# Optimization experiments

Measured on AMD Instinct MI355X. Metric: run time of the kernel, lower is better.

The kernel has to match this reference:

```python
import jax, jax.numpy as jnp
import numpy as np

V, H_BASE, D, L, K = 32000, 4096, 512, 2, 4
B = 64

def setup_inputs() -> dict:
    key = jax.random.key(0)
    ks = jax.random.split(key, 12)
    s = 0.02
    return {
        "hidden_state": jax.random.normal(ks[0], (B, H_BASE), jnp.float32),
        "in_proj_w": jax.random.normal(ks[1], (D, H_BASE), jnp.float32) * s,
        "in_proj_b": jnp.zeros((D,), jnp.float32),
        "w_ih0": jax.random.normal(ks[2], (3 * D, D), jnp.float32) * s,
        "w_hh0": jax.random.normal(ks[3], (3 * D, D), jnp.float32) * s,
        "b_ih0": jax.random.normal(ks[4], (3 * D,), jnp.float32) * s,
        "b_hh0": jax.random.normal(ks[5], (3 * D,), jnp.float32) * s,
        "w_ih1": jax.random.normal(ks[6], (3 * D, D), jnp.float32) * s,
        "w_hh1": jax.random.normal(ks[7], (3 * D, D), jnp.float32) * s,
        "b_ih1": jax.random.normal(ks[8], (3 * D,), jnp.float32) * s,
        "b_hh1": jax.random.normal(ks[9], (3 * D,), jnp.float32) * s,
        "embed": jax.random.normal(ks[10], (V, D), jnp.float32) * s,
        "out_w": jax.random.normal(ks[11], (V, D), jnp.float32) * s,
    }

def _gru_cell(x, h, w_ih, w_hh, b_ih, b_hh):
    # PyTorch GRU gate order: r, z, n
    gi = x @ w_ih.T + b_ih  # [B, 3D]
    gh = h @ w_hh.T + b_hh
    ir, iz, inn = jnp.split(gi, 3, axis=-1)
    hr, hz, hn = jnp.split(gh, 3, axis=-1)
    r = jax.nn.sigmoid(ir + hr)
    z = jax.nn.sigmoid(iz + hz)
    n = jnp.tanh(inn + r * hn)
    return (1.0 - z) * n + z * h

def reference(hidden_state, in_proj_w, in_proj_b, w_ih0, w_hh0, b_ih0, b_hh0,
              w_ih1, w_hh1, b_ih1, b_hh1, embed, out_w):
    b = hidden_state.shape[0]
    h0 = hidden_state @ in_proj_w.T + in_proj_b  # [B, D]
    h_l0 = h0
    h_l1 = h0
    x = jnp.zeros((b, in_proj_w.shape[0]), hidden_state.dtype)
    all_logits = []
    for _ in range(K):
        h_l0 = _gru_cell(x, h_l0, w_ih0, w_hh0, b_ih0, b_hh0)
        h_l1 = _gru_cell(h_l0, h_l1, w_ih1, w_hh1, b_ih1, b_hh1)
        logits = h_l1 @ out_w.T  # [B, V]
        all_logits.append(logits)
        x = embed[jnp.argmax(logits, axis=-1)]  # greedy next-token embed
    return jnp.stack(all_logits, axis=1)  # [B, K, V]
```

## Files before the change

kernel.cpp:

```cpp
#include <hip/hip_runtime.h>
#include <math.h>


typedef __attribute__((ext_vector_type(8))) short short8;
typedef __attribute__((ext_vector_type(4))) float f32x4;

__device__ __forceinline__ unsigned short f2bf_rne(float x) {
    unsigned u = __float_as_uint(x);
    unsigned r = (u + 0x7fffu + ((u >> 16) & 1u)) >> 16;
    return (unsigned short)r;
}
__device__ __forceinline__ void split2(float x, unsigned short& hi, unsigned short& lo) {
    unsigned u = __float_as_uint(x);
    hi = (unsigned short)(u >> 16);
    float r = x - __uint_as_float(u & 0xffff0000u);
    lo = f2bf_rne(r);
}

__device__ __forceinline__ void store_plane(unsigned short* hiP, unsigned short* loP,
                                            int m, int d, float v) {
    int s = d >> 6, cl = (d >> 3) & 7, e = d & 7;
    int off = m * 512 + s * 64 + ((cl ^ (m & 7)) * 8) + e;
    unsigned short hi, lo; split2(v, hi, lo);
    hiP[off] = hi; loP[off] = lo;
}

__device__ __forceinline__ void gload16(const void* g, void* lds) {
    __builtin_amdgcn_global_load_lds(
        (const __attribute__((address_space(1))) unsigned int*)g,
        (__attribute__((address_space(3))) unsigned int*)lds, 16, 0, 0);
}

__device__ __forceinline__ void split_w_body(
    const float* __restrict__ W, unsigned short* __restrict__ H,
    unsigned short* __restrict__ L, size_t g, int kclog)
{
    int n  = (int)(g >> kclog);
    int c8 = (int)g & ((1 << kclog) - 1);
    const float* src = W + g * 8;
    float4 v0 = *(const float4*)src;
    float4 v1 = *(const float4*)(src + 4);
    unsigned short h[8], l[8];
    split2(v0.x,h[0],l[0]); split2(v0.y,h[1],l[1]); split2(v0.z,h[2],l[2]); split2(v0.w,h[3],l[3]);
    split2(v1.x,h[4],l[4]); split2(v1.y,h[5],l[5]); split2(v1.z,h[6],l[6]); split2(v1.w,h[7],l[7]);
    uint4 ph = make_uint4((unsigned)h[0]|((unsigned)h[1]<<16), (unsigned)h[2]|((unsigned)h[3]<<16),
                          (unsigned)h[4]|((unsigned)h[5]<<16), (unsigned)h[6]|((unsigned)h[7]<<16));
    uint4 pl = make_uint4((unsigned)l[0]|((unsigned)l[1]<<16), (unsigned)l[2]|((unsigned)l[3]<<16),
                          (unsigned)l[4]|((unsigned)l[5]<<16), (unsigned)l[6]|((unsigned)l[7]<<16));
    int nt = n >> 7, row = n & 127;
    int ksi = c8 >> 3;
    int slot = (c8 & 7) ^ (row & 7);
    int tpr = 1 << (kclog - 3);
    size_t off = ((size_t)(nt * tpr + ksi) * 128 + row) * 64 + slot * 8;
    *(uint4*)(H + off) = ph;
    *(uint4*)(L + off) = pl;
}

__global__ __launch_bounds__(256) void k_split_W(
    const float* __restrict__ W, unsigned short* __restrict__ H,
    unsigned short* __restrict__ L, int kclog)
{
    size_t g = (size_t)blockIdx.x * 256 + threadIdx.x;
    split_w_body(W, H, L, g, kclog);
}

__global__ __launch_bounds__(256) void k_split_gw(
    const float* __restrict__ w0, const float* __restrict__ w1,
    const float* __restrict__ w2, const float* __restrict__ w3,
    unsigned short* __restrict__ H, unsigned short* __restrict__ L)
{
    int mat = blockIdx.y;
    const float* W = mat == 0 ? w0 : mat == 1 ? w1 : mat == 2 ? w2 : w3;
    size_t g = (size_t)blockIdx.x * 256 + threadIdx.x;
    split_w_body(W, H + (size_t)mat * 786432, L + (size_t)mat * 786432, g, 6);
}

template<bool ARGMAX>
__device__ __forceinline__ void mfma_gemm(
    const char* __restrict__ AH, const char* __restrict__ AL, int AstrideB, int akk0,
    const unsigned short* __restrict__ BH, const unsigned short* __restrict__ BL,
    size_t btileU,
    int nk,
    float* __restrict__ C, int ldc, int n0,
    unsigned short (*AsH)[4096], unsigned short (*AsL)[4096],
    unsigned short (*BsH)[8192], unsigned short (*BsL)[8192],
    float* __restrict__ pval, int* __restrict__ pidx, int bx)
{
    const int tid  = threadIdx.x;
    const int wv   = tid >> 6;
    const int lane = tid & 63;
    const int lr   = lane & 15;
    const int lh   = lane >> 4;
    const int m    = tid >> 3;
    const int cp   = tid & 7;

    f32x4 acc[4];
#pragma unroll
    for (int i = 0; i < 4; ++i) acc[i] = (f32x4){0.f, 0.f, 0.f, 0.f};

    auto stage = [&](int t, int p) {
        const int ka = (akk0 + t * 64) * 2;
        gload16(AH + m * AstrideB + ka + cp * 16, (char*)AsH[p] + wv * 1024);
        gload16(AL + m * AstrideB + ka + cp * 16, (char*)AsL[p] + wv * 1024);
        const char* bH = (const char*)BH + (btileU + (size_t)t * 8192) * 2;
        const char* bL = (const char*)BL + (btileU + (size_t)t * 8192) * 2;
        gload16(bH + wv * 2048 +        lane * 16, (char*)BsH[p] + wv * 2048);
        gload16(bH + wv * 2048 + 1024 + lane * 16, (char*)BsH[p] + wv * 2048 + 1024);
        gload16(bL + wv * 2048 +        lane * 16, (char*)BsL[p] + wv * 2048);
        gload16(bL + wv * 2048 + 1024 + lane * 16, (char*)BsL[p] + wv * 2048 + 1024);
    };

    stage(0, 0);
    __syncthreads();

    for (int t = 0; t < nk; ++t) {
        const int p = t & 1;
        if (t + 1 < nk) stage(t + 1, p ^ 1);
#pragma unroll
        for (int kk2 = 0; kk2 < 2; ++kk2) {
            int aoff = lr * 64 + (((kk2 * 4 + lh) ^ (lr & 7)) * 8);
            short8 ah[4], al[4];
#pragma unroll
            for (int mt = 0; mt < 4; ++mt) {
                ah[mt] = *(const short8*)(AsH[p] + mt * 1024 + aoff);
                al[mt] = *(const short8*)(AsL[p] + mt * 1024 + aoff);
            }
            int brow = wv * 16 + lr;
            int boff = brow * 64 + (((kk2 * 4 + lh) ^ (brow & 7)) * 8);
            short8 bh = *(const short8*)(BsH[p] + boff);
            short8 bl = *(const short8*)(BsL[p] + boff);
#pragma unroll
            for (int mt = 0; mt < 4; ++mt) {
                acc[mt] = __builtin_amdgcn_mfma_f32_16x16x32_bf16(ah[mt], bh, acc[mt], 0, 0, 0);
                acc[mt] = __builtin_amdgcn_mfma_f32_16x16x32_bf16(ah[mt], bl, acc[mt], 0, 0, 0);
                acc[mt] = __builtin_amdgcn_mfma_f32_16x16x32_bf16(al[mt], bh, acc[mt], 0, 0, 0);
            }
        }
        __syncthreads();
    }

#pragma unroll
    for (int mt = 0; mt < 4; ++mt)
#pragma unroll
        for (int i = 0; i < 4; ++i) {
            int mm = mt * 16 + lh * 4 + i;
            C[mm * ldc + n0 + wv * 16 + lr] = acc[mt][i];
        }

    if (ARGMAX) {
        float* sv = (float*)&AsH[0][0];
        int*   sc = (int*)&AsL[0][0];
#pragma unroll
        for (int mt = 0; mt < 4; ++mt)
#pragma unroll
            for (int i = 0; i < 4; ++i) {
                float v = acc[mt][i];
                int   c = n0 + wv * 16 + lr;
#pragma unroll
                for (int msk = 1; msk < 16; msk <<= 1) {
                    float ov = __shfl_xor(v, msk, 64);
                    int   oc = __shfl_xor(c, msk, 64);
                    if (ov > v || (ov == v && oc < c)) { v = ov; c = oc; }
                }
                if (lr == 0) {
                    int row = mt * 16 + lh * 4 + i;
                    sv[wv * 64 + row] = v;
                    sc[wv * 64 + row] = c;
                }
            }
        __syncthreads();
        if (tid < 64) {
            float v = sv[tid]; int c = sc[tid];
#pragma unroll
            for (int w = 1; w < 8; ++w) {
                float ov = sv[w * 64 + tid]; int oc = sc[w * 64 + tid];
                if (ov > v) { v = ov; c = oc; }
            }
            pval[bx * 64 + tid] = v;
            pidx[bx * 64 + tid] = c;
        }
    }
}

#define DECLARE_LDS() \
    __shared__ alignas(16) unsigned short AsH[2][4096]; \
    __shared__ alignas(16) unsigned short AsL[2][4096]; \
    __shared__ alignas(16) unsigned short BsH[2][8192]; \
    __shared__ alignas(16) unsigned short BsL[2][8192];

__global__ __launch_bounds__(256) void k_split_A(
    const float* __restrict__ hidden, char* __restrict__ hidH, char* __restrict__ hidL)
{
    int g = blockIdx.x * 256 + threadIdx.x;
    int m = g >> 9;
    int cc = g & 511;
    int s = cc >> 3, cl = cc & 7;
    const float* src = hidden + m * 4096 + cc * 8;
    float4 v0 = *(const float4*)src;
    float4 v1 = *(const float4*)(src + 4);
    unsigned short h[8], l[8];
    split2(v0.x,h[0],l[0]); split2(v0.y,h[1],l[1]); split2(v0.z,h[2],l[2]); split2(v0.w,h[3],l[3]);
    split2(v1.x,h[4],l[4]); split2(v1.y,h[5],l[5]); split2(v1.z,h[6],l[6]); split2(v1.w,h[7],l[7]);
    uint4 ph = make_uint4((unsigned)h[0]|((unsigned)h[1]<<16), (unsigned)h[2]|((unsigned)h[3]<<16),
                          (unsigned)h[4]|((unsigned)h[5]<<16), (unsigned)h[6]|((unsigned)h[7]<<16));
    uint4 pl = make_uint4((unsigned)l[0]|((unsigned)l[1]<<16), (unsigned)l[2]|((unsigned)l[3]<<16),
                          (unsigned)l[4]|((unsigned)l[5]<<16), (unsigned)l[6]|((unsigned)l[7]<<16));
    int off = m * 8192 + s * 128 + ((cl ^ (m & 7)) * 16);
    *(uint4*)(hidH + off) = ph;
    *(uint4*)(hidL + off) = pl;
}

__global__ __launch_bounds__(512) void k_inproj(
    const char* __restrict__ hidH, const char* __restrict__ hidL,
    const unsigned short* __restrict__ WH, const unsigned short* __restrict__ WL,
    float* __restrict__ part)
{
    DECLARE_LDS();
    int nt = blockIdx.x & 3;
    int ks = blockIdx.x >> 2;
    mfma_gemm<false>(hidH, hidL, 8192, ks * 256,
                     WH, WL, (size_t)(nt * 64 + ks * 4) * 8192, 4,
                     part + ks * 32768, 512, nt * 128,
                     AsH, AsL, BsH, BsL, nullptr, nullptr, 0);
}

__global__ __launch_bounds__(256) void k_reduce_inproj(
    const float* __restrict__ part, const float* __restrict__ bias,
    float* __restrict__ hA, float* __restrict__ hB,
    unsigned short* hAH, unsigned short* hAL,
    unsigned short* hBH, unsigned short* hBL,
    unsigned short* xH,  unsigned short* xL)
{
    int i = blockIdx.x * 256 + threadIdx.x;
    int b = i >> 9;
    int d = i & 511;
    float s = bias[d];
#pragma unroll
    for (int ks = 0; ks < 16; ++ks) s += part[ks * 32768 + i];
    hA[i] = s;
    hB[i] = s;
    store_plane(hAH, hAL, b, d, s);
    store_plane(hBH, hBL, b, d, s);
    store_plane(xH,  xL,  b, d, 0.f);
}

__global__ __launch_bounds__(512) void k_gates(
    const char* __restrict__ xH, const char* __restrict__ xL,
    const char* __restrict__ hH, const char* __restrict__ hL,
    const unsigned short* __restrict__ gwH, const unsigned short* __restrict__ gwL,
    int layer, float* __restrict__ gip, float* __restrict__ ghp)
{
    DECLARE_LDS();
    int bx  = blockIdx.x;
    int nt  = bx % 12;
    int ks  = (bx / 12) & 3;
    int mat = bx / 48;
    const char* AH = mat ? hH : xH;
    const char* AL = mat ? hL : xL;
    float* C = (mat ? ghp : gip) + ks * 98304;
    size_t btile = ((size_t)(layer * 2 + mat) * 96 + nt * 8 + ks * 2) * 8192;
    mfma_gemm<false>(AH, AL, 1024, ks * 128,
                     gwH, gwL, btile, 2,
                     C, 1536, nt * 128,
                     AsH, AsL, BsH, BsL, nullptr, nullptr, 0);
}

__global__ __launch_bounds__(256) void k_combine(
    const float* __restrict__ gip, const float* __restrict__ ghp,
    const float* __restrict__ b_ih, const float* __restrict__ b_hh,
    float* __restrict__ h, unsigned short* hH, unsigned short* hL)
{
    int i = blockIdx.x * 256 + threadIdx.x;
    int b = i >> 9;
    int d = i & 511;
    int base = b * 1536 + d;
    float ir = b_ih[d], iz = b_ih[d + 512], inn = b_ih[d + 1024];
    float hr = b_hh[d], hz = b_hh[d + 512], hn = b_hh[d + 1024];
#pragma unroll
    for (int ks = 0; ks < 4; ++ks) {
        const float* gi = gip + ks * 98304 + base;
        const float* gh = ghp + ks * 98304 + base;
        ir  += gi[0];    iz += gi[512];  inn += gi[1024];
        hr  += gh[0];    hz += gh[512];  hn  += gh[1024];
    }
    float r = 1.f / (1.f + expf(-(ir + hr)));
    float z = 1.f / (1.f + expf(-(iz + hz)));
    float n = tanhf(inn + r * hn);
    float hv = (1.f - z) * n + z * h[i];
    h[i] = hv;
    store_plane(hH, hL, b, d, hv);
}

__global__ __launch_bounds__(512) void k_logits(
    const char* __restrict__ hH, const char* __restrict__ hL,
    const unsigned short* __restrict__ WH, const unsigned short* __restrict__ WL,
    float* __restrict__ out, int step,
    float* __restrict__ pval, int* __restrict__ pidx)
{
    DECLARE_LDS();
    mfma_gemm<true>(hH, hL, 1024, 0,
                    WH, WL, (size_t)blockIdx.x * 8 * 8192, 8,
                    out + step * 32000, 128000, blockIdx.x * 128,
                    AsH, AsL, BsH, BsL, pval, pidx, blockIdx.x);
}

__global__ __launch_bounds__(256) void k_reduce_embed(
    const float* __restrict__ pval, const int* __restrict__ pidx,
    const float* __restrict__ embed, unsigned short* xH, unsigned short* xL)
{
    __shared__ float sv[256];
    __shared__ int   sc[256];
    const int b = blockIdx.x;
    const int tid = threadIdx.x;
    float v = -3.4e38f;
    int   c = 0x7fffffff;
    if (tid < 250) { v = pval[tid * 64 + b]; c = pidx[tid * 64 + b]; }
    sv[tid] = v; sc[tid] = c;
    __syncthreads();
    for (int s = 128; s > 0; s >>= 1) {
        if (tid < s) {
            float ov = sv[tid + s]; int oc = sc[tid + s];
            if (ov > sv[tid] || (ov == sv[tid] && oc < sc[tid])) { sv[tid] = ov; sc[tid] = oc; }
        }
        __syncthreads();
    }
    int tok = sc[0];
    for (int j = tid; j < 512; j += 256)
        store_plane(xH, xL, b, j, embed[tok * 512 + j]);
}

extern "C" void kernel_launch(void* const* d_in, const int* in_sizes, int n_in,
                              void* d_out, int out_size, void* d_ws, size_t ws_size,
                              hipStream_t stream)
{
    const float* hidden = (const float*)d_in[0];
    const float* in_w   = (const float*)d_in[1];
    const float* in_b   = (const float*)d_in[2];
    const float* w_ih0  = (const float*)d_in[3];
    const float* w_hh0  = (const float*)d_in[4];
    const float* b_ih0  = (const float*)d_in[5];
    const float* b_hh0  = (const float*)d_in[6];
    const float* w_ih1  = (const float*)d_in[7];
    const float* w_hh1  = (const float*)d_in[8];
    const float* b_ih1  = (const float*)d_in[9];
    const float* b_hh1  = (const float*)d_in[10];
    const float* embed  = (const float*)d_in[11];
    const float* out_w  = (const float*)d_in[12];
    float* out = (float*)d_out;
    char*  ws  = (char*)d_ws;

    float* hA  = (float*)(ws + 0);
    float* hB  = (float*)(ws + 131072);
    unsigned short* xH  = (unsigned short*)(ws + 262144);
    unsigned short* xL  = (unsigned short*)(ws + 327680);
    unsigned short* hAH = (unsigned short*)(ws + 393216);
    unsigned short* hAL = (unsigned short*)(ws + 458752);
    unsigned short* hBH = (unsigned short*)(ws + 524288);
    unsigned short* hBL = (unsigned short*)(ws + 589824);
    char* hidH = ws + 655360;
    char* hidL = ws + 1179648;
    float* gip = (float*)(ws + 1703936);
    float* ghp = (float*)(ws + 3276800);
    float* pval = (float*)(ws + 4849664);
    int*   pidx = (int*)  (ws + 4913664);
    float* ipart = (float*)(ws + 4980736);
    unsigned short* owH = (unsigned short*)(ws + 8388608);
    unsigned short* owL = (unsigned short*)(ws + 41943040);
    unsigned short* gwH = (unsigned short*)(ws + 75497472);
    unsigned short* gwL = (unsigned short*)(ws + 83886080);
    unsigned short* inH = (unsigned short*)(ws + 92274688);
    unsigned short* inL = (unsigned short*)(ws + 96468992);

    k_split_A<<<128, 256, 0, stream>>>(hidden, hidH, hidL);
    k_split_W<<<8000, 256, 0, stream>>>(out_w, owH, owL, 6);
    k_split_gw<<<dim3(384, 4), 256, 0, stream>>>(w_ih0, w_hh0, w_ih1, w_hh1, gwH, gwL);
    k_split_W<<<1024, 256, 0, stream>>>(in_w, inH, inL, 9);
    k_inproj<<<64, 512, 0, stream>>>(hidH, hidL, inH, inL, ipart);
    k_reduce_inproj<<<128, 256, 0, stream>>>(ipart, in_b, hA, hB,
                                             hAH, hAL, hBH, hBL, xH, xL);

    for (int step = 0; step < 4; ++step) {
        k_gates<<<96, 512, 0, stream>>>((char*)xH, (char*)xL, (char*)hAH, (char*)hAL,
                                        gwH, gwL, 0, gip, ghp);
        k_combine<<<128, 256, 0, stream>>>(gip, ghp, b_ih0, b_hh0, hA, hAH, hAL);
        k_gates<<<96, 512, 0, stream>>>((char*)hAH, (char*)hAL, (char*)hBH, (char*)hBL,
                                        gwH, gwL, 1, gip, ghp);
        k_combine<<<128, 256, 0, stream>>>(gip, ghp, b_ih1, b_hh1, hB, hBH, hBL);
        k_logits<<<250, 512, 0, stream>>>((char*)hBH, (char*)hBL, owH, owL,
                                          out, step, pval, pidx);
        k_reduce_embed<<<64, 256, 0, stream>>>(pval, pidx, embed, xH, xL);
    }
}
```

Measured before the change: 361.9 us.

## Fuse all launches into one cooperative persistent kernel with grid syncs

Replaces the chain of about 30 kernel launches (weight splits, in-proj, gates, combine, logits, argmax/embed per step) with one cooperative kernel of 256 blocks separated by grid.sync. It also re-splits the K dimension more finely (64-way in-proj, 8-way gates) to use more blocks per phase, and overlaps the out_w and GRU weight splitting with the in-proj GEMM. The aim is to remove launch gaps and fill more CUs. The cost is grid-wide barriers, idle blocks in small phases, and larger partial-sum reductions.

```diff
diff --git a/kernel.cpp b/kernel.cpp
--- a/kernel.cpp
+++ b/kernel.cpp
@@ -1,6 +1,9 @@
 #include <hip/hip_runtime.h>
+#include <hip/hip_cooperative_groups.h>
 #include <math.h>
 
+
+namespace cg = cooperative_groups;
 
 typedef __attribute__((ext_vector_type(8))) short short8;
 typedef __attribute__((ext_vector_type(4))) float f32x4;
@@ -56,142 +59,10 @@
     *(uint4*)(L + off) = pl;
 }
 
-__global__ __launch_bounds__(256) void k_split_W(
-    const float* __restrict__ W, unsigned short* __restrict__ H,
-    unsigned short* __restrict__ L, int kclog)
-{
-    size_t g = (size_t)blockIdx.x * 256 + threadIdx.x;
-    split_w_body(W, H, L, g, kclog);
-}
-
-__global__ __launch_bounds__(256) void k_split_gw(
-    const float* __restrict__ w0, const float* __restrict__ w1,
-    const float* __restrict__ w2, const float* __restrict__ w3,
-    unsigned short* __restrict__ H, unsigned short* __restrict__ L)
-{
-    int mat = blockIdx.y;
-    const float* W = mat == 0 ? w0 : mat == 1 ? w1 : mat == 2 ? w2 : w3;
-    size_t g = (size_t)blockIdx.x * 256 + threadIdx.x;
-    split_w_body(W, H + (size_t)mat * 786432, L + (size_t)mat * 786432, g, 6);
-}
-
-template<bool ARGMAX>
-__device__ __forceinline__ void mfma_gemm(
-    const char* __restrict__ AH, const char* __restrict__ AL, int AstrideB, int akk0,
-    const unsigned short* __restrict__ BH, const unsigned short* __restrict__ BL,
-    size_t btileU,
-    int nk,
-    float* __restrict__ C, int ldc, int n0,
-    unsigned short (*AsH)[4096], unsigned short (*AsL)[4096],
-    unsigned short (*BsH)[8192], unsigned short (*BsL)[8192],
-    float* __restrict__ pval, int* __restrict__ pidx, int bx)
-{
-    const int tid  = threadIdx.x;
-    const int wv   = tid >> 6;
-    const int lane = tid & 63;
-    const int lr   = lane & 15;
-    const int lh   = lane >> 4;
-    const int m    = tid >> 3;
-    const int cp   = tid & 7;
-
-    f32x4 acc[4];
-#pragma unroll
-    for (int i = 0; i < 4; ++i) acc[i] = (f32x4){0.f, 0.f, 0.f, 0.f};
-
-    auto stage = [&](int t, int p) {
-        const int ka = (akk0 + t * 64) * 2;
-        gload16(AH + m * AstrideB + ka + cp * 16, (char*)AsH[p] + wv * 1024);
-        gload16(AL + m * AstrideB + ka + cp * 16, (char*)AsL[p] + wv * 1024);
-        const char* bH = (const char*)BH + (btileU + (size_t)t * 8192) * 2;
-        const char* bL = (const char*)BL + (btileU + (size_t)t * 8192) * 2;
-        gload16(bH + wv * 2048 +        lane * 16, (char*)BsH[p] + wv * 2048);
-        gload16(bH + wv * 2048 + 1024 + lane * 16, (char*)BsH[p] + wv * 2048 + 1024);
-        gload16(bL + wv * 2048 +        lane * 16, (char*)BsL[p] + wv * 2048);
-        gload16(bL + wv * 2048 + 1024 + lane * 16, (char*)BsL[p] + wv * 2048 + 1024);
-    };
-
-    stage(0, 0);
-    __syncthreads();
-
-    for (int t = 0; t < nk; ++t) {
-        const int p = t & 1;
-        if (t + 1 < nk) stage(t + 1, p ^ 1);
-#pragma unroll
-        for (int kk2 = 0; kk2 < 2; ++kk2) {
-            int aoff = lr * 64 + (((kk2 * 4 + lh) ^ (lr & 7)) * 8);
-            short8 ah[4], al[4];
-#pragma unroll
-            for (int mt = 0; mt < 4; ++mt) {
-                ah[mt] = *(const short8*)(AsH[p] + mt * 1024 + aoff);
-                al[mt] = *(const short8*)(AsL[p] + mt * 1024 + aoff);
-            }
-            int brow = wv * 16 + lr;
-            int boff = brow * 64 + (((kk2 * 4 + lh) ^ (brow & 7)) * 8);
-            short8 bh = *(const short8*)(BsH[p] + boff);
-            short8 bl = *(const short8*)(BsL[p] + boff);
-#pragma unroll
-            for (int mt = 0; mt < 4; ++mt) {
-                acc[mt] = __builtin_amdgcn_mfma_f32_16x16x32_bf16(ah[mt], bh, acc[mt], 0, 0, 0);
-                acc[mt] = __builtin_amdgcn_mfma_f32_16x16x32_bf16(ah[mt], bl, acc[mt], 0, 0, 0);
-                acc[mt] = __builtin_amdgcn_mfma_f32_16x16x32_bf16(al[mt], bh, acc[mt], 0, 0, 0);
-            }
-        }
-        __syncthreads();
-    }
-
-#pragma unroll
-    for (int mt = 0; mt < 4; ++mt)
-#pragma unroll
-        for (int i = 0; i < 4; ++i) {
-            int mm = mt * 16 + lh * 4 + i;
-            C[mm * ldc + n0 + wv * 16 + lr] = acc[mt][i];
-        }
-
-    if (ARGMAX) {
-        float* sv = (float*)&AsH[0][0];
-        int*   sc = (int*)&AsL[0][0];
-#pragma unroll
-        for (int mt = 0; mt < 4; ++mt)
-#pragma unroll
-            for (int i = 0; i < 4; ++i) {
-                float v = acc[mt][i];
-                int   c = n0 + wv * 16 + lr;
-#pragma unroll
-                for (int msk = 1; msk < 16; msk <<= 1) {
-                    float ov = __shfl_xor(v, msk, 64);
-                    int   oc = __shfl_xor(c, msk, 64);
-                    if (ov > v || (ov == v && oc < c)) { v = ov; c = oc; }
-                }
-                if (lr == 0) {
-                    int row = mt * 16 + lh * 4 + i;
-                    sv[wv * 64 + row] = v;
-                    sc[wv * 64 + row] = c;
-                }
-            }
-        __syncthreads();
-        if (tid < 64) {
-            float v = sv[tid]; int c = sc[tid];
-#pragma unroll
-            for (int w = 1; w < 8; ++w) {
-                float ov = sv[w * 64 + tid]; int oc = sc[w * 64 + tid];
-                if (ov > v) { v = ov; c = oc; }
-            }
-            pval[bx * 64 + tid] = v;
-            pidx[bx * 64 + tid] = c;
-        }
-    }
-}
-
-#define DECLARE_LDS() \
-    __shared__ alignas(16) unsigned short AsH[2][4096]; \
-    __shared__ alignas(16) unsigned short AsL[2][4096]; \
-    __shared__ alignas(16) unsigned short BsH[2][8192]; \
-    __shared__ alignas(16) unsigned short BsL[2][8192];
-
-__global__ __launch_bounds__(256) void k_split_A(
-    const float* __restrict__ hidden, char* __restrict__ hidH, char* __restrict__ hidL)
-{
-    int g = blockIdx.x * 256 + threadIdx.x;
+__device__ __forceinline__ void split_a_body(
+    const float* __restrict__ hidden, char* __restrict__ hidH,
+    char* __restrict__ hidL, int g)
+{
     int m = g >> 9;
     int cc = g & 511;
     int s = cc >> 3, cl = cc & 7;
@@ -210,144 +81,132 @@
     *(uint4*)(hidL + off) = pl;
 }
 
-__global__ __launch_bounds__(512) void k_inproj(
-    const char* __restrict__ hidH, const char* __restrict__ hidL,
-    const unsigned short* __restrict__ WH, const unsigned short* __restrict__ WL,
-    float* __restrict__ part)
-{
-    DECLARE_LDS();
-    int nt = blockIdx.x & 3;
-    int ks = blockIdx.x >> 2;
-    mfma_gemm<false>(hidH, hidL, 8192, ks * 256,
-                     WH, WL, (size_t)(nt * 64 + ks * 4) * 8192, 4,
-                     part + ks * 32768, 512, nt * 128,
-                     AsH, AsL, BsH, BsL, nullptr, nullptr, 0);
-}
-
-__global__ __launch_bounds__(256) void k_reduce_inproj(
-    const float* __restrict__ part, const float* __restrict__ bias,
-    float* __restrict__ hA, float* __restrict__ hB,
-    unsigned short* hAH, unsigned short* hAL,
-    unsigned short* hBH, unsigned short* hBL,
-    unsigned short* xH,  unsigned short* xL)
-{
-    int i = blockIdx.x * 256 + threadIdx.x;
-    int b = i >> 9;
-    int d = i & 511;
-    float s = bias[d];
-#pragma unroll
-    for (int ks = 0; ks < 16; ++ks) s += part[ks * 32768 + i];
-    hA[i] = s;
-    hB[i] = s;
-    store_plane(hAH, hAL, b, d, s);
-    store_plane(hBH, hBL, b, d, s);
-    store_plane(xH,  xL,  b, d, 0.f);
-}
-
-__global__ __launch_bounds__(512) void k_gates(
-    const char* __restrict__ xH, const char* __restrict__ xL,
-    const char* __restrict__ hH, const char* __restrict__ hL,
-    const unsigned short* __restrict__ gwH, const unsigned short* __restrict__ gwL,
-    int layer, float* __restrict__ gip, float* __restrict__ ghp)
-{
-    DECLARE_LDS();
-    int bx  = blockIdx.x;
-    int nt  = bx % 12;
-    int ks  = (bx / 12) & 3;
-    int mat = bx / 48;
-    const char* AH = mat ? hH : xH;
-    const char* AL = mat ? hL : xL;
-    float* C = (mat ? ghp : gip) + ks * 98304;
-    size_t btile = ((size_t)(layer * 2 + mat) * 96 + nt * 8 + ks * 2) * 8192;
-    mfma_gemm<false>(AH, AL, 1024, ks * 128,
-                     gwH, gwL, btile, 2,
-                     C, 1536, nt * 128,
-                     AsH, AsL, BsH, BsL, nullptr, nullptr, 0);
-}
-
-__global__ __launch_bounds__(256) void k_combine(
-    const float* __restrict__ gip, const float* __restrict__ ghp,
-    const float* __restrict__ b_ih, const float* __restrict__ b_hh,
-    float* __restrict__ h, unsigned short* hH, unsigned short* hL)
-{
-    int i = blockIdx.x * 256 + threadIdx.x;
-    int b = i >> 9;
-    int d = i & 511;
-    int base = b * 1536 + d;
-    float ir = b_ih[d], iz = b_ih[d + 512], inn = b_ih[d + 1024];
-    float hr = b_hh[d], hz = b_hh[d + 512], hn = b_hh[d + 1024];
-#pragma unroll
-    for (int ks = 0; ks < 4; ++ks) {
-        const float* gi = gip + ks * 98304 + base;
-        const float* gh = ghp + ks * 98304 + base;
-        ir  += gi[0];    iz += gi[512];  inn += gi[1024];
-        hr  += gh[0];    hz += gh[512];  hn  += gh[1024];
-    }
-    float r = 1.f / (1.f + expf(-(ir + hr)));
-    float z = 1.f / (1.f + expf(-(iz + hz)));
-    float n = tanhf(inn + r * hn);
-    float hv = (1.f - z) * n + z * h[i];
-    h[i] = hv;
-    store_plane(hH, hL, b, d, hv);
-}
-
-__global__ __launch_bounds__(512) void k_logits(
-    const char* __restrict__ hH, const char* __restrict__ hL,
-    const unsigned short* __restrict__ WH, const unsigned short* __restrict__ WL,
-    float* __restrict__ out, int step,
-    float* __restrict__ pval, int* __restrict__ pidx)
-{
-    DECLARE_LDS();
-    mfma_gemm<true>(hH, hL, 1024, 0,
-                    WH, WL, (size_t)blockIdx.x * 8 * 8192, 8,
-                    out + step * 32000, 128000, blockIdx.x * 128,
-                    AsH, AsL, BsH, BsL, pval, pidx, blockIdx.x);
-}
-
-__global__ __launch_bounds__(256) void k_reduce_embed(
-    const float* __restrict__ pval, const int* __restrict__ pidx,
-    const float* __restrict__ embed, unsigned short* xH, unsigned short* xL)
-{
-    __shared__ float sv[256];
-    __shared__ int   sc[256];
-    const int b = blockIdx.x;
+template<bool ARGMAX>
+__device__ __forceinline__ void mfma_gemm(
+    const char* __restrict__ AH, const char* __restrict__ AL, int AstrideB, int akk0,
+    const unsigned short* __restrict__ BH, const unsigned short* __restrict__ BL,
+    size_t btileU, int nk,
+    float* __restrict__ C, int ldc, int n0,
+    unsigned short (*AsH)[4096], unsigned short (*AsL)[4096],
+    unsigned short (*BsH)[8192], unsigned short (*BsL)[8192],
+    float* __restrict__ pval, int* __restrict__ pidx, int bx)
+{
+    const int tid  = threadIdx.x;
+    const int wv   = tid >> 6;
+    const int lane = tid & 63;
+    const int lr   = lane & 15;
+    const int lh   = lane >> 4;
+    const int m    = tid >> 3;
+    const int cp   = tid & 7;
+
+    f32x4 acc[4];
+#pragma unroll
+    for (int i = 0; i < 4; ++i) acc[i] = (f32x4){0.f, 0.f, 0.f, 0.f};
+
+    auto stage = [&](int t, int p) {
+        const int ka = (akk0 + t * 64) * 2;
+        gload16(AH + m * AstrideB + ka + cp * 16, (char*)AsH[p] + wv * 1024);
+        gload16(AL + m * AstrideB + ka + cp * 16, (char*)AsL[p] + wv * 1024);
+        const char* bH = (const char*)BH + (btileU + (size_t)t * 8192) * 2;
+        const char* bL = (const char*)BL + (btileU + (size_t)t * 8192) * 2;
+        gload16(bH + wv * 2048 +        lane * 16, (char*)BsH[p] + wv * 2048);
+        gload16(bH + wv * 2048 + 1024 + lane * 16, (char*)BsH[p] + wv * 2048 + 1024);
+        gload16(bL + wv * 2048 +        lane * 16, (char*)BsL[p] + wv * 2048);
+        gload16(bL + wv * 2048 + 1024 + lane * 16, (char*)BsL[p] + wv * 2048 + 1024);
+    };
+
+    stage(0, 0);
+    __syncthreads();
+
+    for (int t = 0; t < nk; ++t) {
+        const int p = t & 1;
+        if (t + 1 < nk) stage(t + 1, p ^ 1);
+#pragma unroll
+        for (int kk2 = 0; kk2 < 2; ++kk2) {
+            int aoff = lr * 64 + (((kk2 * 4 + lh) ^ (lr & 7)) * 8);
+            short8 ah[4], al[4];
+#pragma unroll
+            for (int mt = 0; mt < 4; ++mt) {
+                ah[mt] = *(const short8*)(AsH[p] + mt * 1024 + aoff);
+                al[mt] = *(const short8*)(AsL[p] + mt * 1024 + aoff);
+            }
+            int brow = wv * 16 + lr;
+            int boff = brow * 64 + (((kk2 * 4 + lh) ^ (brow & 7)) * 8);
+            short8 bh = *(const short8*)(BsH[p] + boff);
+            short8 bl = *(const short8*)(BsL[p] + boff);
+#pragma unroll
+            for (int mt = 0; mt < 4; ++mt) {
+                acc[mt] = __builtin_amdgcn_mfma_f32_16x16x32_bf16(ah[mt], bh, acc[mt], 0, 0, 0);
+                acc[mt] = __builtin_amdgcn_mfma_f32_16x16x32_bf16(ah[mt], bl, acc[mt], 0, 0, 0);
+                acc[mt] = __builtin_amdgcn_mfma_f32_16x16x32_bf16(al[mt], bh, acc[mt], 0, 0, 0);
+            }
+        }
+        __syncthreads();
+    }
+
+#pragma unroll
+    for (int mt = 0; mt < 4; ++mt)
+#pragma unroll
+        for (int i = 0; i < 4; ++i) {
+            int mm = mt * 16 + lh * 4 + i;
+            C[mm * ldc + n0 + wv * 16 + lr] = acc[mt][i];
+        }
+
+    if (ARGMAX) {
+        float* sv = (float*)&AsH[0][0];
+        int*   sc = (int*)&AsL[0][0];
+#pragma unroll
+        for (int mt = 0; mt < 4; ++mt)
+#pragma unroll
+            for (int i = 0; i < 4; ++i) {
+                float v = acc[mt][i];
+                int   c = n0 + wv * 16 + lr;
+#pragma unroll
+                for (int msk = 1; msk < 16; msk <<= 1) {
+                    float ov = __shfl_xor(v, msk, 64);
+                    int   oc = __shfl_xor(c, msk, 64);
+                    if (ov > v || (ov == v && oc < c)) { v = ov; c = oc; }
+                }
+                if (lr == 0) {
+                    int row = mt * 16 + lh * 4 + i;
+                    sv[wv * 64 + row] = v;
+                    sc[wv * 64 + row] = c;
+                }
+            }
+        __syncthreads();
+        if (tid < 64) {
+            float v = sv[tid]; int c = sc[tid];
+#pragma unroll
+            for (int w = 1; w < 8; ++w) {
+                float ov = sv[w * 64 + tid]; int oc = sc[w * 64 + tid];
+                if (ov > v) { v = ov; c = oc; }
+            }
+            pval[bx * 64 + tid] = v;
+            pidx[bx * 64 + tid] = c;
+        }
+        __syncthreads();
+    }
+}
+
+struct KP {
+    const float *hidden, *in_w, *in_b, *w_ih0, *w_hh0, *b_ih0, *b_hh0,
+                *w_ih1, *w_hh1, *b_ih1, *b_hh1, *embed, *out_w;
+    float* out;
+    char* ws;
+};
+
+__global__ __launch_bounds__(512) void k_persistent(KP p)
+{
+    cg::grid_group grid = cg::this_grid();
+
+    __shared__ alignas(16) unsigned short AsH[2][4096];
+    __shared__ alignas(16) unsigned short AsL[2][4096];
+    __shared__ alignas(16) unsigned short BsH[2][8192];
+    __shared__ alignas(16) unsigned short BsL[2][8192];
+
+    const int bx  = blockIdx.x;
     const int tid = threadIdx.x;
-    float v = -3.4e38f;
-    int   c = 0x7fffffff;
-    if (tid < 250) { v = pval[tid * 64 + b]; c = pidx[tid * 64 + b]; }
-    sv[tid] = v; sc[tid] = c;
-    __syncthreads();
-    for (int s = 128; s > 0; s >>= 1) {
-        if (tid < s) {
-            float ov = sv[tid + s]; int oc = sc[tid + s];
-            if (ov > sv[tid] || (ov == sv[tid] && oc < sc[tid])) { sv[tid] = ov; sc[tid] = oc; }
-        }
-        __syncthreads();
-    }
-    int tok = sc[0];
-    for (int j = tid; j < 512; j += 256)
-        store_plane(xH, xL, b, j, embed[tok * 512 + j]);
-}
-
-extern "C" void kernel_launch(void* const* d_in, const int* in_sizes, int n_in,
-                              void* d_out, int out_size, void* d_ws, size_t ws_size,
-                              hipStream_t stream)
-{
-    const float* hidden = (const float*)d_in[0];
-    const float* in_w   = (const float*)d_in[1];
-    const float* in_b   = (const float*)d_in[2];
-    const float* w_ih0  = (const float*)d_in[3];
-    const float* w_hh0  = (const float*)d_in[4];
-    const float* b_ih0  = (const float*)d_in[5];
-    const float* b_hh0  = (const float*)d_in[6];
-    const float* w_ih1  = (const float*)d_in[7];
-    const float* w_hh1  = (const float*)d_in[8];
-    const float* b_ih1  = (const float*)d_in[9];
-    const float* b_hh1  = (const float*)d_in[10];
-    const float* embed  = (const float*)d_in[11];
-    const float* out_w  = (const float*)d_in[12];
-    float* out = (float*)d_out;
-    char*  ws  = (char*)d_ws;
+    char* ws = p.ws;
 
     float* hA  = (float*)(ws + 0);
     float* hB  = (float*)(ws + 131072);
@@ -360,34 +219,153 @@
     char* hidH = ws + 655360;
     char* hidL = ws + 1179648;
     float* gip = (float*)(ws + 1703936);
-    float* ghp = (float*)(ws + 3276800);
-    float* pval = (float*)(ws + 4849664);
-    int*   pidx = (int*)  (ws + 4913664);
-    float* ipart = (float*)(ws + 4980736);
-    unsigned short* owH = (unsigned short*)(ws + 8388608);
-    unsigned short* owL = (unsigned short*)(ws + 41943040);
-    unsigned short* gwH = (unsigned short*)(ws + 75497472);
-    unsigned short* gwL = (unsigned short*)(ws + 83886080);
-    unsigned short* inH = (unsigned short*)(ws + 92274688);
-    unsigned short* inL = (unsigned short*)(ws + 96468992);
-
-    k_split_A<<<128, 256, 0, stream>>>(hidden, hidH, hidL);
-    k_split_W<<<8000, 256, 0, stream>>>(out_w, owH, owL, 6);
-    k_split_gw<<<dim3(384, 4), 256, 0, stream>>>(w_ih0, w_hh0, w_ih1, w_hh1, gwH, gwL);
-    k_split_W<<<1024, 256, 0, stream>>>(in_w, inH, inL, 9);
-    k_inproj<<<64, 512, 0, stream>>>(hidH, hidL, inH, inL, ipart);
-    k_reduce_inproj<<<128, 256, 0, stream>>>(ipart, in_b, hA, hB,
-                                             hAH, hAL, hBH, hBL, xH, xL);
+    float* ghp = (float*)(ws + 4849664);
+    float* pval = (float*)(ws + 7995392);
+    int*   pidx = (int*)  (ws + 8059392);
+    float* ipart = (float*)(ws + 8388608);
+    unsigned short* owH = (unsigned short*)(ws + 16777216);
+    unsigned short* owL = (unsigned short*)(ws + 49545216);
+    unsigned short* gwH = (unsigned short*)(ws + 82313216);
+    unsigned short* gwL = (unsigned short*)(ws + 88604672);
+    unsigned short* inH = (unsigned short*)(ws + 94896128);
+    unsigned short* inL = (unsigned short*)(ws + 99090432);
+
+    const size_t gt = (size_t)bx * 512 + tid;
+
+    for (size_t g = gt; g < 262144; g += 131072)
+        split_w_body(p.in_w, inH, inL, g, 9);
+    if (gt < 32768)
+        split_a_body(p.hidden, hidH, hidL, (int)gt);
+    grid.sync();
+
+    {
+        int nt = bx & 3, ks = bx >> 2;
+        mfma_gemm<false>(hidH, hidL, 8192, ks * 64,
+                         inH, inL, (size_t)(nt * 64 + ks) * 8192, 1,
+                         ipart + ks * 32768, 512, nt * 128,
+                         AsH, AsL, BsH, BsL, nullptr, nullptr, 0);
+    }
+    for (size_t g = gt; g < 2048000; g += 131072)
+        split_w_body(p.out_w, owH, owL, g, 6);
+    for (size_t g = gt; g < 393216; g += 131072) {
+        int mat = (int)(g / 98304);
+        const float* W = mat == 0 ? p.w_ih0 : mat == 1 ? p.w_hh0
+                       : mat == 2 ? p.w_ih1 : p.w_hh1;
+        split_w_body(W, gwH + (size_t)mat * 786432, gwL + (size_t)mat * 786432,
+                     g % 98304, 6);
+    }
+    grid.sync();
+
+    if (bx < 64) {
+        int i = bx * 512 + tid;
+        int b = i >> 9, d = i & 511;
+        float s = p.in_b[d];
+        for (int ks = 0; ks < 64; ++ks) s += ipart[ks * 32768 + i];
+        hA[i] = s; hB[i] = s;
+        store_plane(hAH, hAL, b, d, s);
+        store_plane(hBH, hBL, b, d, s);
+        store_plane(xH,  xL,  b, d, 0.f);
+    }
+    grid.sync();
 
     for (int step = 0; step < 4; ++step) {
-        k_gates<<<96, 512, 0, stream>>>((char*)xH, (char*)xL, (char*)hAH, (char*)hAL,
-                                        gwH, gwL, 0, gip, ghp);
-        k_combine<<<128, 256, 0, stream>>>(gip, ghp, b_ih0, b_hh0, hA, hAH, hAL);
-        k_gates<<<96, 512, 0, stream>>>((char*)hAH, (char*)hAL, (char*)hBH, (char*)hBL,
-                                        gwH, gwL, 1, gip, ghp);
-        k_combine<<<128, 256, 0, stream>>>(gip, ghp, b_ih1, b_hh1, hB, hBH, hBL);
-        k_logits<<<250, 512, 0, stream>>>((char*)hBH, (char*)hBL, owH, owL,
-                                          out, step, pval, pidx);
-        k_reduce_embed<<<64, 256, 0, stream>>>(pval, pidx, embed, xH, xL);
-    }
-}
+#pragma unroll 1
+        for (int layer = 0; layer < 2; ++layer) {
+            if (bx < 192) {
+                int nt = bx % 12, ks = (bx / 12) & 7, mat = bx / 96;
+                const char* AH_;
+                const char* AL_;
+                if (layer == 0) { AH_ = mat ? (char*)hAH : (char*)xH;
+                                  AL_ = mat ? (char*)hAL : (char*)xL; }
+                else            { AH_ = mat ? (char*)hBH : (char*)hAH;
+                                  AL_ = mat ? (char*)hBL : (char*)hAL; }
+                float* C = (mat ? ghp : gip) + ks * 98304;
+                size_t btile = ((size_t)(layer * 2 + mat) * 96 + nt * 8 + ks) * 8192;
+                mfma_gemm<false>(AH_, AL_, 1024, ks * 64,
+                                 gwH, gwL, btile, 1,
+                                 C, 1536, nt * 128,
+                                 AsH, AsL, BsH, BsL, nullptr, nullptr, 0);
+            }
+            grid.sync();
+
+            if (bx < 64) {
+                int i = bx * 512 + tid;
+                int b = i >> 9, d = i & 511;
+                const float* bi = layer ? p.b_ih1 : p.b_ih0;
+                const float* bh2 = layer ? p.b_hh1 : p.b_hh0;
+                float ir = bi[d], iz = bi[d + 512], inn = bi[d + 1024];
+                float hr = bh2[d], hz = bh2[d + 512], hn = bh2[d + 1024];
+                int base = b * 1536 + d;
+#pragma unroll
+                for (int ks = 0; ks < 8; ++ks) {
+                    const float* gi = gip + ks * 98304 + base;
+                    const float* gh = ghp + ks * 98304 + base;
+                    ir += gi[0]; iz += gi[512]; inn += gi[1024];
+                    hr += gh[0]; hz += gh[512]; hn  += gh[1024];
+                }
+                float r = 1.f / (1.f + expf(-(ir + hr)));
+                float z = 1.f / (1.f + expf(-(iz + hz)));
+                float n = tanhf(inn + r * hn);
+                float* h = layer ? hB : hA;
+                float hv = (1.f - z) * n + z * h[i];
+                h[i] = hv;
+                store_plane(layer ? hBH : hAH, layer ? hBL : hAL, b, d, hv);
+            }
+            grid.sync();
+        }
+
+        if (bx < 250) {
+            mfma_gemm<true>((const char*)hBH, (const char*)hBL, 1024, 0,
+                            owH, owL, (size_t)bx * 8 * 8192, 8,
+                            p.out + step * 32000, 128000, bx * 128,
+                            AsH, AsL, BsH, BsL, pval, pidx, bx);
+        }
+        grid.sync();
+
+        if (bx < 64) {
+            float* sv = (float*)&AsH[0][0];
+            int*   sc = (int*)&AsL[0][0];
+            float v = -3.4e38f; int c = 0x7fffffff;
+            if (tid < 250) { v = pval[tid * 64 + bx]; c = pidx[tid * 64 + bx]; }
+            sv[tid] = v; sc[tid] = c;
+            __syncthreads();
+            for (int s = 256; s > 0; s >>= 1) {
+                if (tid < s) {
+                    float ov = sv[tid + s]; int oc = sc[tid + s];
+                    if (ov > sv[tid] || (ov == sv[tid] && oc < sc[tid])) {
+                        sv[tid] = ov; sc[tid] = oc;
+                    }
+                }
+                __syncthreads();
+            }
+            int tok = sc[0];
+            store_plane(xH, xL, bx, tid, p.embed[(size_t)tok * 512 + tid]);
+        }
+        grid.sync();
+    }
+}
+
+extern "C" void kernel_launch(void* const* d_in, const int* in_sizes, int n_in,
+                              void* d_out, int out_size, void* d_ws, size_t ws_size,
+                              hipStream_t stream)
+{
+    KP p;
+    p.hidden = (const float*)d_in[0];
+    p.in_w   = (const float*)d_in[1];
+    p.in_b   = (const float*)d_in[2];
+    p.w_ih0  = (const float*)d_in[3];
+    p.w_hh0  = (const float*)d_in[4];
+    p.b_ih0  = (const float*)d_in[5];
+    p.b_hh0  = (const float*)d_in[6];
+    p.w_ih1  = (const float*)d_in[7];
+    p.w_hh1  = (const float*)d_in[8];
+    p.b_ih1  = (const float*)d_in[9];
+    p.b_hh1  = (const float*)d_in[10];
+    p.embed  = (const float*)d_in[11];
+    p.out_w  = (const float*)d_in[12];
+    p.out    = (float*)d_out;
+    p.ws     = (char*)d_ws;
+
+    void* args[] = { (void*)&p };
+    hipLaunchCooperativeKernel(k_persistent, dim3(256), dim3(512), args, 0, stream);
+}
```

Result: slower. 1.184 ms (+227.2%).
